# Performance work log

Measured on AMD Instinct MI355X. Metric: run time of the kernel, lower is better.

Reference implementation:

```python
import jax, jax.numpy as jnp
import numpy as np

N_NODES = 50000
N_EDGES = 640000
IN_FEATS = 128
OUT_FEATS = 64
K = 2  # number of sparse sum-aggregation hops


def setup_inputs() -> dict:
    key = jax.random.key(0)
    k1, k2, k3, k4, k5 = jax.random.split(key, 5)
    features = jax.random.normal(k1, (N_NODES, IN_FEATS), dtype=jnp.float32)
    src = jax.random.randint(k2, (N_EDGES,), 0, N_NODES, dtype=jnp.int64)
    dst = jax.random.randint(k3, (N_EDGES,), 0, N_NODES, dtype=jnp.int64)
    weight = jax.random.normal(k4, (IN_FEATS, OUT_FEATS), dtype=jnp.float32) * (IN_FEATS ** -0.5)
    bias = jax.random.normal(k5, (OUT_FEATS,), dtype=jnp.float32) * 0.02
    return {"features": features, "src": src, "dst": dst, "weight": weight, "bias": bias}


def reference(features, src, dst, weight, bias):
    N = features.shape[0]
    ones = jnp.ones(src.shape[0], dtype=features.dtype)
    # degrees (graph is static across hops)
    out_deg = jax.ops.segment_sum(ones, src, num_segments=N)  # out-degree of each node
    in_deg = jax.ops.segment_sum(ones, dst, num_segments=N)   # in-degree of each node
    norm_src = jax.lax.rsqrt(jnp.clip(out_deg, 1.0))[:, None]
    norm_dst = jax.lax.rsqrt(jnp.clip(in_deg, 1.0))[:, None]

    # K hops of unnormalized copy_u/sum message passing
    h = features
    for _ in range(K):
        h = jax.ops.segment_sum(h[src], dst, num_segments=N)

    # GraphConv with norm='both': D_in^{-1/2} A^T D_out^{-1/2} h W + b
    h = h * norm_src
    h = h @ weight  # in_feats > out_feats: project before aggregating
    h = jax.ops.segment_sum(h[src], dst, num_segments=N)
    h = h * norm_dst + bias
    return h
```

## Files before the change

kernel.cpp:

```cpp
#include <hip/hip_runtime.h>
#include <hip/hip_bf16.h>

#define IN_FEATS 128
#define OUT_FEATS 64
#define HB_D 128
#define HB_S 64
#define PB 256
#define MAX_WORDS 12544
#define SMEM_U32 12544
#define PROJ_NODES 256
#define HOP_BLOCKS 2048

static inline char* align_up(char* p, size_t a) {
    return (char*)(((uintptr_t)p + a - 1) & ~(uintptr_t)(a - 1));
}

__device__ __forceinline__ unsigned pack_bf16(float a, float b) {
    unsigned ua = __float_as_uint(a), ub = __float_as_uint(b);
    ua = (ua + 0x7fffu + ((ua >> 16) & 1u)) >> 16;
    ub = (ub + 0x7fffu + ((ub >> 16) & 1u)) >> 16;
    return ua | (ub << 16);
}
__device__ __forceinline__ float bf16_lo(unsigned u) { return __uint_as_float(u << 16); }
__device__ __forceinline__ float bf16_hi(unsigned u) { return __uint_as_float(u & 0xffff0000u); }

__global__ __launch_bounds__(1024)
void hist_proj_kernel(const int* __restrict__ src, const int* __restrict__ dst,
                      const float* __restrict__ X, const float* __restrict__ W,
                      unsigned* __restrict__ partial, uint2* __restrict__ Y,
                      int* __restrict__ gcounter,
                      int N, int E, int slice_d, int slice_s, int words) {
    __shared__ unsigned smem[SMEM_U32];
    int tid = (int)threadIdx.x;
    int b = (int)blockIdx.x;

    if (b == 0 && tid == 0) *gcounter = 0;

    if (b < HB_D + HB_S) {
        unsigned* h = smem;
        for (int w = tid; w < words; w += 1024) h[w] = 0u;
        __syncthreads();
        const int* __restrict__ keys;
        int sb, se;
        if (b < HB_D) { keys = dst; sb = b * slice_d; se = min(sb + slice_d, E); }
        else          { keys = src; sb = (b - HB_D) * slice_s; se = min(sb + slice_s, E); }
        for (int i = sb + tid * 4; i < se; i += 1024 * 4) {
            if (i + 3 < se) {
                int4 k4 = *reinterpret_cast<const int4*>(keys + i);
                atomicAdd(&h[k4.x >> 2], 1u << ((k4.x & 3) * 8));
                atomicAdd(&h[k4.y >> 2], 1u << ((k4.y & 3) * 8));
                atomicAdd(&h[k4.z >> 2], 1u << ((k4.z & 3) * 8));
                atomicAdd(&h[k4.w >> 2], 1u << ((k4.w & 3) * 8));
            } else {
                for (int j = i; j < se; ++j) {
                    int k = keys[j];
                    atomicAdd(&h[k >> 2], 1u << ((k & 3) * 8));
                }
            }
        }
        __syncthreads();
        unsigned* __restrict__ outp = partial + (size_t)b * words;
        for (int w = tid; w < words; w += 1024) outp[w] = h[w];
    } else {
        float* w_s = (float*)smem;
        for (int i = tid; i < IN_FEATS * OUT_FEATS / 4; i += 1024)
            reinterpret_cast<float4*>(w_s)[i] = reinterpret_cast<const float4*>(W)[i];
        __syncthreads();
        int slot = tid >> 4;
        int jj = (tid & 15) * 4;
        int n0 = (b - (HB_D + HB_S)) * PROJ_NODES + slot * 4;
        int m0 = min(n0 + 0, N - 1), m1 = min(n0 + 1, N - 1);
        int m2 = min(n0 + 2, N - 1), m3 = min(n0 + 3, N - 1);
        const float* __restrict__ x0p = X + (size_t)m0 * IN_FEATS;
        const float* __restrict__ x1p = X + (size_t)m1 * IN_FEATS;
        const float* __restrict__ x2p = X + (size_t)m2 * IN_FEATS;
        const float* __restrict__ x3p = X + (size_t)m3 * IN_FEATS;
        float4 a0 = make_float4(0.f, 0.f, 0.f, 0.f), a1 = a0, a2 = a0, a3 = a0;
#pragma unroll 2
        for (int k = 0; k < IN_FEATS; k += 4) {
            float4 x0 = *reinterpret_cast<const float4*>(x0p + k);
            float4 x1 = *reinterpret_cast<const float4*>(x1p + k);
            float4 x2 = *reinterpret_cast<const float4*>(x2p + k);
            float4 x3 = *reinterpret_cast<const float4*>(x3p + k);
#pragma unroll
            for (int q = 0; q < 4; ++q) {
                float4 w = *reinterpret_cast<const float4*>(&w_s[(k + q) * OUT_FEATS + jj]);
                float e0 = (q == 0) ? x0.x : (q == 1) ? x0.y : (q == 2) ? x0.z : x0.w;
                float e1 = (q == 0) ? x1.x : (q == 1) ? x1.y : (q == 2) ? x1.z : x1.w;
                float e2 = (q == 0) ? x2.x : (q == 1) ? x2.y : (q == 2) ? x2.z : x2.w;
                float e3 = (q == 0) ? x3.x : (q == 1) ? x3.y : (q == 2) ? x3.z : x3.w;
                a0.x = fmaf(e0, w.x, a0.x); a0.y = fmaf(e0, w.y, a0.y);
                a0.z = fmaf(e0, w.z, a0.z); a0.w = fmaf(e0, w.w, a0.w);
                a1.x = fmaf(e1, w.x, a1.x); a1.y = fmaf(e1, w.y, a1.y);
                a1.z = fmaf(e1, w.z, a1.z); a1.w = fmaf(e1, w.w, a1.w);
                a2.x = fmaf(e2, w.x, a2.x); a2.y = fmaf(e2, w.y, a2.y);
                a2.z = fmaf(e2, w.z, a2.z); a2.w = fmaf(e2, w.w, a2.w);
                a3.x = fmaf(e3, w.x, a3.x); a3.y = fmaf(e3, w.y, a3.y);
                a3.z = fmaf(e3, w.z, a3.z); a3.w = fmaf(e3, w.w, a3.w);
            }
        }
        float4 accs[4] = {a0, a1, a2, a3};
#pragma unroll
        for (int i = 0; i < 4; ++i) {
            int node = n0 + i;
            if (node < N) {
                uint2 o;
                o.x = pack_bf16(accs[i].x, accs[i].y);
                o.y = pack_bf16(accs[i].z, accs[i].w);
                Y[(size_t)node * (OUT_FEATS / 4) + (jj >> 2)] = o;
            }
        }
    }
}

__global__ __launch_bounds__(PB)
void prefix_alloc_kernel(const unsigned* __restrict__ partial, unsigned* __restrict__ pprefix,
                         int2* __restrict__ rowext, float* __restrict__ normS,
                         float* __restrict__ normD, int* __restrict__ gcounter,
                         int N, int words) {
    __shared__ int tsum[PB];
    __shared__ int s_base;
    int tid = (int)threadIdx.x;
    int w = (int)blockIdx.x * PB + tid;
    unsigned run = 0, ssum = 0;
    if (w < words) {
        for (int bb = 0; bb < HB_D; bb += 16) {
            unsigned v[16], pfx[16];
#pragma unroll
            for (int i = 0; i < 16; ++i) v[i] = partial[(size_t)(bb + i) * words + w];
#pragma unroll
            for (int i = 0; i < 16; ++i) { pfx[i] = run; run += v[i]; }
#pragma unroll
            for (int i = 0; i < 16; ++i) pprefix[(size_t)(bb + i) * words + w] = pfx[i];
        }
        for (int bb = HB_D; bb < HB_D + HB_S; bb += 16) {
            unsigned v[16];
#pragma unroll
            for (int i = 0; i < 16; ++i) v[i] = partial[(size_t)(bb + i) * words + w];
#pragma unroll
            for (int i = 0; i < 16; ++i) ssum += v[i];
        }
    }
    int c0 = (int)(run & 0xffu), c1 = (int)((run >> 8) & 0xffu);
    int c2 = (int)((run >> 16) & 0xffu), c3 = (int)(run >> 24);
    int dtot = c0 + c1 + c2 + c3;
    tsum[tid] = dtot;
    __syncthreads();
    for (int off = 1; off < PB; off <<= 1) {
        int t = (tid >= off) ? tsum[tid - off] : 0;
        __syncthreads();
        tsum[tid] += t;
        __syncthreads();
    }
    if (tid == PB - 1) s_base = atomicAdd(gcounter, tsum[PB - 1]);
    __syncthreads();
    if (w < words) {
        int excl = tsum[tid] - dtot + s_base;
        int r0 = excl, r1 = r0 + c0, r2 = r1 + c1, r3 = r2 + c2;
        int base = 4 * w;
        if (base + 3 < N) {
            int4* re = reinterpret_cast<int4*>(rowext + base);
            re[0] = make_int4(r0, r1, r1, r2);
            re[1] = make_int4(r2, r3, r3, r3 + c3);
            float4 nD = make_float4(rsqrtf(fmaxf((float)c0, 1.f)), rsqrtf(fmaxf((float)c1, 1.f)),
                                    rsqrtf(fmaxf((float)c2, 1.f)), rsqrtf(fmaxf((float)c3, 1.f)));
            int s0 = (int)(ssum & 0xffu), s1 = (int)((ssum >> 8) & 0xffu);
            int s2 = (int)((ssum >> 16) & 0xffu), s3 = (int)(ssum >> 24);
            float4 nS = make_float4(rsqrtf(fmaxf((float)s0, 1.f)), rsqrtf(fmaxf((float)s1, 1.f)),
                                    rsqrtf(fmaxf((float)s2, 1.f)), rsqrtf(fmaxf((float)s3, 1.f)));
            *reinterpret_cast<float4*>(normD + base) = nD;
            *reinterpret_cast<float4*>(normS + base) = nS;
        } else {
            int r[5] = {r0, r1, r2, r3, r3 + c3};
            int cD[4] = {c0, c1, c2, c3};
            int cS[4] = {(int)(ssum & 0xffu), (int)((ssum >> 8) & 0xffu),
                         (int)((ssum >> 16) & 0xffu), (int)(ssum >> 24)};
            for (int i = 0; i < 4 && base + i < N; ++i) {
                rowext[base + i] = make_int2(r[i], r[i + 1]);
                normD[base + i] = rsqrtf(fmaxf((float)cD[i], 1.f));
                normS[base + i] = rsqrtf(fmaxf((float)cS[i], 1.f));
            }
        }
    }
}

__global__ __launch_bounds__(1024)
void fill_kernel(const int* __restrict__ src, const int* __restrict__ dst,
                 const unsigned* __restrict__ pprefix, const int2* __restrict__ rowext,
                 unsigned short* __restrict__ csr16, int E, int slice, int words) {
    __shared__ unsigned cur[MAX_WORDS];
    int tid = (int)threadIdx.x;
    int b = (int)blockIdx.x;
    const unsigned* __restrict__ pp = pprefix + (size_t)b * words;
    for (int w = tid; w < words; w += 1024) cur[w] = pp[w];
    __syncthreads();
    int sb = b * slice;
    int se = min(sb + slice, E);
    for (int i = sb + tid * 4; i < se; i += 1024 * 4) {
        if (i + 3 < se) {
            int4 d4 = *reinterpret_cast<const int4*>(dst + i);
            int4 s4 = *reinterpret_cast<const int4*>(src + i);
            int dd[4] = {d4.x, d4.y, d4.z, d4.w};
            int ss[4] = {s4.x, s4.y, s4.z, s4.w};
#pragma unroll
            for (int j = 0; j < 4; ++j) {
                int bin = dd[j];
                unsigned sh = (unsigned)(bin & 3) * 8u;
                unsigned old = atomicAdd(&cur[bin >> 2], 1u << sh);
                int off = (int)((old >> sh) & 0xffu);
                csr16[rowext[bin].x + off] = (unsigned short)ss[j];
            }
        } else {
            for (int j = i; j < se; ++j) {
                int bin = dst[j];
                unsigned sh = (unsigned)(bin & 3) * 8u;
                unsigned old = atomicAdd(&cur[bin >> 2], 1u << sh);
                int off = (int)((old >> sh) & 0xffu);
                csr16[rowext[bin].x + off] = (unsigned short)src[j];
            }
        }
    }
}

template <int EPI>
__global__ __launch_bounds__(256)
void gather_hop(const uint2* __restrict__ Yin, const int2* __restrict__ rowext,
                const unsigned short* __restrict__ csr16, void* __restrict__ Yout,
                const float* __restrict__ vec, const float* __restrict__ bias,
                int N) {
    int lane = (int)threadIdx.x & 63;
    int g = lane >> 4;
    int ci = lane & 15;
    int gwave = (int)blockIdx.x * 4 + ((int)threadIdx.x >> 6);
    int nwaves = (int)gridDim.x * 4;
    for (int node = gwave; node < N; node += nwaves) {
        int2 be = rowext[node];
        int beg = be.x, end = be.y;
        float4 acc = make_float4(0.f, 0.f, 0.f, 0.f);
        float4 acc2 = make_float4(0.f, 0.f, 0.f, 0.f);
        int k = beg + g;
        for (; k + 4 < end; k += 8) {
            int s0 = (int)csr16[k];
            int s1 = (int)csr16[k + 4];
            uint2 v0 = Yin[(size_t)s0 * (OUT_FEATS / 4) + ci];
            uint2 v1 = Yin[(size_t)s1 * (OUT_FEATS / 4) + ci];
            acc.x += bf16_lo(v0.x); acc.y += bf16_hi(v0.x);
            acc.z += bf16_lo(v0.y); acc.w += bf16_hi(v0.y);
            acc2.x += bf16_lo(v1.x); acc2.y += bf16_hi(v1.x);
            acc2.z += bf16_lo(v1.y); acc2.w += bf16_hi(v1.y);
        }
        if (k < end) {
            uint2 v = Yin[(size_t)csr16[k] * (OUT_FEATS / 4) + ci];
            acc.x += bf16_lo(v.x); acc.y += bf16_hi(v.x);
            acc.z += bf16_lo(v.y); acc.w += bf16_hi(v.y);
        }
        acc.x += acc2.x; acc.y += acc2.y; acc.z += acc2.z; acc.w += acc2.w;
        acc.x += __shfl_xor(acc.x, 16); acc.y += __shfl_xor(acc.y, 16);
        acc.z += __shfl_xor(acc.z, 16); acc.w += __shfl_xor(acc.w, 16);
        acc.x += __shfl_xor(acc.x, 32); acc.y += __shfl_xor(acc.y, 32);
        acc.z += __shfl_xor(acc.z, 32); acc.w += __shfl_xor(acc.w, 32);
        if (g == 0) {
            if (EPI == 1) {
                float sc = vec[node];
                acc.x *= sc; acc.y *= sc; acc.z *= sc; acc.w *= sc;
            }
            if (EPI == 2) {
                float sc = vec[node];
                float4 bb = *reinterpret_cast<const float4*>(bias + ci * 4);
                acc.x = fmaf(acc.x, sc, bb.x); acc.y = fmaf(acc.y, sc, bb.y);
                acc.z = fmaf(acc.z, sc, bb.z); acc.w = fmaf(acc.w, sc, bb.w);
                reinterpret_cast<float4*>(Yout)[(size_t)node * (OUT_FEATS / 4) + ci] = acc;
            } else {
                uint2 o;
                o.x = pack_bf16(acc.x, acc.y);
                o.y = pack_bf16(acc.z, acc.w);
                reinterpret_cast<uint2*>(Yout)[(size_t)node * (OUT_FEATS / 4) + ci] = o;
            }
        }
    }
}

extern "C" void kernel_launch(void* const* d_in, const int* in_sizes, int n_in,
                              void* d_out, int out_size, void* d_ws, size_t ws_size,
                              hipStream_t stream) {
    const float* features = (const float*)d_in[0];
    const int*   src      = (const int*)d_in[1];
    const int*   dst      = (const int*)d_in[2];
    const float* weight   = (const float*)d_in[3];
    const float* bias     = (const float*)d_in[4];

    const int N = in_sizes[0] / IN_FEATS;
    const int E = in_sizes[1];
    const int words = (N + 3) / 4;
    const int NB = (words + PB - 1) / PB;
    const int slice_d = (((E + HB_D - 1) / HB_D) + 3) & ~3;
    const int slice_s = (((E + HB_S - 1) / HB_S) + 3) & ~3;
    const int projBlocks = (N + PROJ_NODES - 1) / PROJ_NODES;

    char* p = (char*)d_ws;
    float* normS   = (float*)p;  p = align_up(p + sizeof(float) * (N + 4), 256);
    float* normD   = (float*)p;  p = align_up(p + sizeof(float) * (N + 4), 256);
    uint2* y0      = (uint2*)p;  p = align_up(p + sizeof(uint2) * (size_t)N * (OUT_FEATS / 4), 256);
    uint2* y1      = (uint2*)p;  p = align_up(p + sizeof(uint2) * (size_t)N * (OUT_FEATS / 4), 256);
    int2*  rowext  = (int2*)p;   p = align_up(p + sizeof(int2) * (N + 4), 256);
    int*   gcounter= (int*)p;    p = align_up(p + sizeof(int) * 4, 256);
    unsigned short* csr16 = (unsigned short*)p;  p = align_up(p + sizeof(unsigned short) * (size_t)E, 256);
    unsigned* partial = (unsigned*)p;  p = align_up(p + sizeof(unsigned) * (size_t)(HB_D + HB_S) * words, 256);
    unsigned* pprefix = (unsigned*)p;  p = align_up(p + sizeof(unsigned) * (size_t)HB_D * words, 256);

    float* out = (float*)d_out;

    hist_proj_kernel<<<HB_D + HB_S + projBlocks, 1024, 0, stream>>>(
        src, dst, features, weight, partial, y0, gcounter, N, E, slice_d, slice_s, words);
    prefix_alloc_kernel<<<NB, PB, 0, stream>>>(partial, pprefix, rowext, normS, normD,
                                               gcounter, N, words);
    fill_kernel<<<HB_D, 1024, 0, stream>>>(src, dst, pprefix, rowext, csr16, E, slice_d, words);

    const int hop_blocks = min((N + 3) / 4, HOP_BLOCKS);
    gather_hop<0><<<hop_blocks, 256, 0, stream>>>(y0, rowext, csr16, (void*)y1, nullptr, nullptr, N);
    gather_hop<1><<<hop_blocks, 256, 0, stream>>>(y1, rowext, csr16, (void*)y0, normS, nullptr, N);
    gather_hop<2><<<hop_blocks, 256, 0, stream>>>(y0, rowext, csr16, (void*)out, normD, bias, N);
}
```

Baseline: 109.6 us.

## Fuse prefix, CSR fill, and three gather hops into one cooperative kernel

Result: slower. 265.8 us (+142.5%).

```diff
diff --git a/kernel.cpp b/kernel.cpp
--- a/kernel.cpp
+++ b/kernel.cpp
@@ -1,15 +1,18 @@
 #include <hip/hip_runtime.h>
 #include <hip/hip_bf16.h>
+#include <hip/hip_cooperative_groups.h>
+
+namespace cg = cooperative_groups;
 
 #define IN_FEATS 128
 #define OUT_FEATS 64
 #define HB_D 128
 #define HB_S 64
-#define PB 256
 #define MAX_WORDS 12544
 #define SMEM_U32 12544
 #define PROJ_NODES 256
-#define HOP_BLOCKS 2048
+#define COOP_BLOCKS 256
+#define COOP_THREADS 1024
 
 static inline char* align_up(char* p, size_t a) {
     return (char*)(((uintptr_t)p + a - 1) & ~(uintptr_t)(a - 1));
@@ -113,126 +116,18 @@
     }
 }
 
-__global__ __launch_bounds__(PB)
-void prefix_alloc_kernel(const unsigned* __restrict__ partial, unsigned* __restrict__ pprefix,
-                         int2* __restrict__ rowext, float* __restrict__ normS,
-                         float* __restrict__ normD, int* __restrict__ gcounter,
-                         int N, int words) {
-    __shared__ int tsum[PB];
-    __shared__ int s_base;
-    int tid = (int)threadIdx.x;
-    int w = (int)blockIdx.x * PB + tid;
-    unsigned run = 0, ssum = 0;
-    if (w < words) {
-        for (int bb = 0; bb < HB_D; bb += 16) {
-            unsigned v[16], pfx[16];
-#pragma unroll
-            for (int i = 0; i < 16; ++i) v[i] = partial[(size_t)(bb + i) * words + w];
-#pragma unroll
-            for (int i = 0; i < 16; ++i) { pfx[i] = run; run += v[i]; }
-#pragma unroll
-            for (int i = 0; i < 16; ++i) pprefix[(size_t)(bb + i) * words + w] = pfx[i];
-        }
-        for (int bb = HB_D; bb < HB_D + HB_S; bb += 16) {
-            unsigned v[16];
-#pragma unroll
-            for (int i = 0; i < 16; ++i) v[i] = partial[(size_t)(bb + i) * words + w];
-#pragma unroll
-            for (int i = 0; i < 16; ++i) ssum += v[i];
-        }
-    }
-    int c0 = (int)(run & 0xffu), c1 = (int)((run >> 8) & 0xffu);
-    int c2 = (int)((run >> 16) & 0xffu), c3 = (int)(run >> 24);
-    int dtot = c0 + c1 + c2 + c3;
-    tsum[tid] = dtot;
-    __syncthreads();
-    for (int off = 1; off < PB; off <<= 1) {
-        int t = (tid >= off) ? tsum[tid - off] : 0;
-        __syncthreads();
-        tsum[tid] += t;
-        __syncthreads();
-    }
-    if (tid == PB - 1) s_base = atomicAdd(gcounter, tsum[PB - 1]);
-    __syncthreads();
-    if (w < words) {
-        int excl = tsum[tid] - dtot + s_base;
-        int r0 = excl, r1 = r0 + c0, r2 = r1 + c1, r3 = r2 + c2;
-        int base = 4 * w;
-        if (base + 3 < N) {
-            int4* re = reinterpret_cast<int4*>(rowext + base);
-            re[0] = make_int4(r0, r1, r1, r2);
-            re[1] = make_int4(r2, r3, r3, r3 + c3);
-            float4 nD = make_float4(rsqrtf(fmaxf((float)c0, 1.f)), rsqrtf(fmaxf((float)c1, 1.f)),
-                                    rsqrtf(fmaxf((float)c2, 1.f)), rsqrtf(fmaxf((float)c3, 1.f)));
-            int s0 = (int)(ssum & 0xffu), s1 = (int)((ssum >> 8) & 0xffu);
-            int s2 = (int)((ssum >> 16) & 0xffu), s3 = (int)(ssum >> 24);
-            float4 nS = make_float4(rsqrtf(fmaxf((float)s0, 1.f)), rsqrtf(fmaxf((float)s1, 1.f)),
-                                    rsqrtf(fmaxf((float)s2, 1.f)), rsqrtf(fmaxf((float)s3, 1.f)));
-            *reinterpret_cast<float4*>(normD + base) = nD;
-            *reinterpret_cast<float4*>(normS + base) = nS;
-        } else {
-            int r[5] = {r0, r1, r2, r3, r3 + c3};
-            int cD[4] = {c0, c1, c2, c3};
-            int cS[4] = {(int)(ssum & 0xffu), (int)((ssum >> 8) & 0xffu),
-                         (int)((ssum >> 16) & 0xffu), (int)(ssum >> 24)};
-            for (int i = 0; i < 4 && base + i < N; ++i) {
-                rowext[base + i] = make_int2(r[i], r[i + 1]);
-                normD[base + i] = rsqrtf(fmaxf((float)cD[i], 1.f));
-                normS[base + i] = rsqrtf(fmaxf((float)cS[i], 1.f));
-            }
-        }
-    }
-}
-
-__global__ __launch_bounds__(1024)
-void fill_kernel(const int* __restrict__ src, const int* __restrict__ dst,
-                 const unsigned* __restrict__ pprefix, const int2* __restrict__ rowext,
-                 unsigned short* __restrict__ csr16, int E, int slice, int words) {
-    __shared__ unsigned cur[MAX_WORDS];
-    int tid = (int)threadIdx.x;
-    int b = (int)blockIdx.x;
-    const unsigned* __restrict__ pp = pprefix + (size_t)b * words;
-    for (int w = tid; w < words; w += 1024) cur[w] = pp[w];
-    __syncthreads();
-    int sb = b * slice;
-    int se = min(sb + slice, E);
-    for (int i = sb + tid * 4; i < se; i += 1024 * 4) {
-        if (i + 3 < se) {
-            int4 d4 = *reinterpret_cast<const int4*>(dst + i);
-            int4 s4 = *reinterpret_cast<const int4*>(src + i);
-            int dd[4] = {d4.x, d4.y, d4.z, d4.w};
-            int ss[4] = {s4.x, s4.y, s4.z, s4.w};
-#pragma unroll
-            for (int j = 0; j < 4; ++j) {
-                int bin = dd[j];
-                unsigned sh = (unsigned)(bin & 3) * 8u;
-                unsigned old = atomicAdd(&cur[bin >> 2], 1u << sh);
-                int off = (int)((old >> sh) & 0xffu);
-                csr16[rowext[bin].x + off] = (unsigned short)ss[j];
-            }
-        } else {
-            for (int j = i; j < se; ++j) {
-                int bin = dst[j];
-                unsigned sh = (unsigned)(bin & 3) * 8u;
-                unsigned old = atomicAdd(&cur[bin >> 2], 1u << sh);
-                int off = (int)((old >> sh) & 0xffu);
-                csr16[rowext[bin].x + off] = (unsigned short)src[j];
-            }
-        }
-    }
-}
-
 template <int EPI>
-__global__ __launch_bounds__(256)
-void gather_hop(const uint2* __restrict__ Yin, const int2* __restrict__ rowext,
-                const unsigned short* __restrict__ csr16, void* __restrict__ Yout,
-                const float* __restrict__ vec, const float* __restrict__ bias,
-                int N) {
+__device__ __forceinline__ void hop_body(const uint2* __restrict__ Yin,
+                                         const int2* __restrict__ rowext,
+                                         const unsigned short* __restrict__ csr16,
+                                         void* __restrict__ Yout,
+                                         const float* __restrict__ vec,
+                                         const float* __restrict__ bias, int N) {
     int lane = (int)threadIdx.x & 63;
     int g = lane >> 4;
     int ci = lane & 15;
-    int gwave = (int)blockIdx.x * 4 + ((int)threadIdx.x >> 6);
-    int nwaves = (int)gridDim.x * 4;
+    int gwave = (int)blockIdx.x * (COOP_THREADS / 64) + ((int)threadIdx.x >> 6);
+    int nwaves = (int)gridDim.x * (COOP_THREADS / 64);
     for (int node = gwave; node < N; node += nwaves) {
         int2 be = rowext[node];
         int beg = be.x, end = be.y;
@@ -280,6 +175,137 @@
     }
 }
 
+__global__ __launch_bounds__(COOP_THREADS)
+void build_hops_kernel(const int* __restrict__ src, const int* __restrict__ dst,
+                       const unsigned* __restrict__ partial, unsigned* __restrict__ pprefix,
+                       int2* __restrict__ rowext, float* __restrict__ normS,
+                       float* __restrict__ normD, int* __restrict__ gcounter,
+                       unsigned short* __restrict__ csr16,
+                       const uint2* __restrict__ y0, uint2* __restrict__ y1,
+                       float* __restrict__ out, const float* __restrict__ bias,
+                       int N, int E, int slice_d, int words) {
+    cg::grid_group grid = cg::this_grid();
+    __shared__ unsigned smem[SMEM_U32];
+    __shared__ int s_base;
+    int tid = (int)threadIdx.x;
+    int b = (int)blockIdx.x;
+
+    {
+        const int NBc = (words + 255) / 256;
+        int w = -1;
+        unsigned run = 0, ssum = 0;
+        int dtot = 0;
+        if (b < NBc && tid < 256) {
+            w = b * 256 + tid;
+            if (w < words) {
+                for (int bb = 0; bb < HB_D; bb += 16) {
+                    unsigned v[16], pfx[16];
+#pragma unroll
+                    for (int i = 0; i < 16; ++i) v[i] = partial[(size_t)(bb + i) * words + w];
+#pragma unroll
+                    for (int i = 0; i < 16; ++i) { pfx[i] = run; run += v[i]; }
+#pragma unroll
+                    for (int i = 0; i < 16; ++i) pprefix[(size_t)(bb + i) * words + w] = pfx[i];
+                }
+                for (int bb = HB_D; bb < HB_D + HB_S; bb += 16) {
+                    unsigned v[16];
+#pragma unroll
+                    for (int i = 0; i < 16; ++i) v[i] = partial[(size_t)(bb + i) * words + w];
+#pragma unroll
+                    for (int i = 0; i < 16; ++i) ssum += v[i];
+                }
+            } else {
+                w = -1;
+            }
+        }
+        int c0 = (int)(run & 0xffu), c1 = (int)((run >> 8) & 0xffu);
+        int c2 = (int)((run >> 16) & 0xffu), c3 = (int)(run >> 24);
+        dtot = c0 + c1 + c2 + c3;
+        int* tsum = (int*)smem;
+        if (tid < 256) tsum[tid] = dtot;
+        __syncthreads();
+        for (int off = 1; off < 256; off <<= 1) {
+            int t = 0;
+            if (tid < 256 && tid >= off) t = tsum[tid - off];
+            __syncthreads();
+            if (tid < 256) tsum[tid] += t;
+            __syncthreads();
+        }
+        if (b < NBc && tid == 255) s_base = atomicAdd(gcounter, tsum[255]);
+        __syncthreads();
+        if (w >= 0) {
+            int excl = tsum[tid] - dtot + s_base;
+            int r0 = excl, r1 = r0 + c0, r2 = r1 + c1, r3 = r2 + c2;
+            int base = 4 * w;
+            if (base + 3 < N) {
+                int4* re = reinterpret_cast<int4*>(rowext + base);
+                re[0] = make_int4(r0, r1, r1, r2);
+                re[1] = make_int4(r2, r3, r3, r3 + c3);
+                float4 nD = make_float4(rsqrtf(fmaxf((float)c0, 1.f)), rsqrtf(fmaxf((float)c1, 1.f)),
+                                        rsqrtf(fmaxf((float)c2, 1.f)), rsqrtf(fmaxf((float)c3, 1.f)));
+                int s0 = (int)(ssum & 0xffu), s1 = (int)((ssum >> 8) & 0xffu);
+                int s2 = (int)((ssum >> 16) & 0xffu), s3 = (int)(ssum >> 24);
+                float4 nS = make_float4(rsqrtf(fmaxf((float)s0, 1.f)), rsqrtf(fmaxf((float)s1, 1.f)),
+                                        rsqrtf(fmaxf((float)s2, 1.f)), rsqrtf(fmaxf((float)s3, 1.f)));
+                *reinterpret_cast<float4*>(normD + base) = nD;
+                *reinterpret_cast<float4*>(normS + base) = nS;
+            } else {
+                int r[5] = {r0, r1, r2, r3, r3 + c3};
+                int cD[4] = {c0, c1, c2, c3};
+                int cS[4] = {(int)(ssum & 0xffu), (int)((ssum >> 8) & 0xffu),
+                             (int)((ssum >> 16) & 0xffu), (int)(ssum >> 24)};
+                for (int i = 0; i < 4 && base + i < N; ++i) {
+                    rowext[base + i] = make_int2(r[i], r[i + 1]);
+                    normD[base + i] = rsqrtf(fmaxf((float)cD[i], 1.f));
+                    normS[base + i] = rsqrtf(fmaxf((float)cS[i], 1.f));
+                }
+            }
+        }
+    }
+    grid.sync();
+
+    if (b < HB_D) {
+        const unsigned* __restrict__ pp = pprefix + (size_t)b * words;
+        for (int w = tid; w < words; w += COOP_THREADS) smem[w] = pp[w];
+    }
+    __syncthreads();
+    if (b < HB_D) {
+        int sb = b * slice_d;
+        int se = min(sb + slice_d, E);
+        for (int i = sb + tid * 4; i < se; i += COOP_THREADS * 4) {
+            if (i + 3 < se) {
+                int4 d4 = *reinterpret_cast<const int4*>(dst + i);
+                int4 s4 = *reinterpret_cast<const int4*>(src + i);
+                int dd[4] = {d4.x, d4.y, d4.z, d4.w};
+                int ss[4] = {s4.x, s4.y, s4.z, s4.w};
+#pragma unroll
+                for (int j = 0; j < 4; ++j) {
+                    int bin = dd[j];
+                    unsigned sh = (unsigned)(bin & 3) * 8u;
+                    unsigned old = atomicAdd(&smem[bin >> 2], 1u << sh);
+                    int off = (int)((old >> sh) & 0xffu);
+                    csr16[rowext[bin].x + off] = (unsigned short)ss[j];
+                }
+            } else {
+                for (int j = i; j < se; ++j) {
+                    int bin = dst[j];
+                    unsigned sh = (unsigned)(bin & 3) * 8u;
+                    unsigned old = atomicAdd(&smem[bin >> 2], 1u << sh);
+                    int off = (int)((old >> sh) & 0xffu);
+                    csr16[rowext[bin].x + off] = (unsigned short)src[j];
+                }
+            }
+        }
+    }
+    grid.sync();
+
+    hop_body<0>(y0, rowext, csr16, (void*)y1, nullptr, nullptr, N);
+    grid.sync();
+    hop_body<1>(y1, rowext, csr16, (void*)const_cast<uint2*>(y0), normS, nullptr, N);
+    grid.sync();
+    hop_body<2>(y0, rowext, csr16, (void*)out, normD, bias, N);
+}
+
 extern "C" void kernel_launch(void* const* d_in, const int* in_sizes, int n_in,
                               void* d_out, int out_size, void* d_ws, size_t ws_size,
                               hipStream_t stream) {
@@ -292,7 +318,6 @@
     const int N = in_sizes[0] / IN_FEATS;
     const int E = in_sizes[1];
     const int words = (N + 3) / 4;
-    const int NB = (words + PB - 1) / PB;
     const int slice_d = (((E + HB_D - 1) / HB_D) + 3) & ~3;
     const int slice_s = (((E + HB_S - 1) / HB_S) + 3) & ~3;
     const int projBlocks = (N + PROJ_NODES - 1) / PROJ_NODES;
@@ -312,12 +337,16 @@
 
     hist_proj_kernel<<<HB_D + HB_S + projBlocks, 1024, 0, stream>>>(
         src, dst, features, weight, partial, y0, gcounter, N, E, slice_d, slice_s, words);
-    prefix_alloc_kernel<<<NB, PB, 0, stream>>>(partial, pprefix, rowext, normS, normD,
-                                               gcounter, N, words);
-    fill_kernel<<<HB_D, 1024, 0, stream>>>(src, dst, pprefix, rowext, csr16, E, slice_d, words);
-
-    const int hop_blocks = min((N + 3) / 4, HOP_BLOCKS);
-    gather_hop<0><<<hop_blocks, 256, 0, stream>>>(y0, rowext, csr16, (void*)y1, nullptr, nullptr, N);
-    gather_hop<1><<<hop_blocks, 256, 0, stream>>>(y1, rowext, csr16, (void*)y0, normS, nullptr, N);
-    gather_hop<2><<<hop_blocks, 256, 0, stream>>>(y0, rowext, csr16, (void*)out, normD, bias, N);
-}
+
+    {
+        void* args[] = {
+            (void*)&src, (void*)&dst, (void*)&partial, (void*)&pprefix,
+            (void*)&rowext, (void*)&normS, (void*)&normD, (void*)&gcounter,
+            (void*)&csr16, (void*)&y0, (void*)&y1, (void*)&out, (void*)&bias,
+            (void*)&N, (void*)&E, (void*)&slice_d, (void*)&words
+        };
+        hipLaunchCooperativeKernel((const void*)build_hops_kernel,
+                                   dim3(COOP_BLOCKS), dim3(COOP_THREADS),
+                                   args, 0, stream);
+    }
+}
```
